# Optimization experiments

Hardware: AMD Instinct MI355X
Metric: run time of the kernel (lower is better)

The kernel has to match this reference:

```python
import jax, jax.numpy as jnp
import numpy as np

# static config (matches init_kwargs)
PL, LAT, LON = 8, 48, 96
WP, WL, WW = 2, 6, 12
SP, SL, SN = 1, 3, 6
NH = 16


def _earth_position_index(ws):
    wp, wl, ww = ws
    zi = np.arange(wp); zj = -np.arange(wp) * wp
    hi = np.arange(wl); hj = -np.arange(wl) * wl
    w = np.arange(ww)
    c1 = np.stack(np.meshgrid(zi, hi, w, indexing='ij')).reshape(3, -1)
    c2 = np.stack(np.meshgrid(zj, hj, w, indexing='ij')).reshape(3, -1)
    coords = (c1[:, :, None] - c2[:, None, :]).transpose(1, 2, 0).astype(np.int64)
    coords[:, :, 2] += ww - 1
    coords[:, :, 1] *= 2 * ww - 1
    coords[:, :, 0] *= (2 * ww - 1) * wl * wl
    return coords.sum(-1)  # (N, N)

_POS_IDX = jnp.asarray(_earth_position_index((WP, WL, WW)))


def _ln(x, w, b, eps=1e-5):
    m = x.mean(-1, keepdims=True)
    v = x.var(-1, keepdims=True)
    return (x - m) / jnp.sqrt(v + eps) * w + b


def setup_inputs() -> dict:
    key = jax.random.key(0)
    ks = jax.random.split(key, 8)
    B, C = 1, 512
    L = PL * LAT * LON
    TOW = (PL // WP) * (LAT // WL)
    TBL = WP * WP * WL * WL * (2 * WW - 1)
    s = 0.02
    return {
        'x': jax.random.normal(ks[0], (B, L, C), jnp.float32),
        'norm1_w': jnp.ones((C,), jnp.float32), 'norm1_b': jnp.zeros((C,), jnp.float32),
        'qkv_w': jax.random.normal(ks[1], (C, 3 * C), jnp.float32) * s,
        'qkv_b': jnp.zeros((3 * C,), jnp.float32),
        'proj_w': jax.random.normal(ks[2], (C, C), jnp.float32) * s,
        'proj_b': jnp.zeros((C,), jnp.float32),
        'bias_table': jax.random.normal(ks[3], (TBL, TOW, NH), jnp.float32) * s,
        'norm2_w': jnp.ones((C,), jnp.float32), 'norm2_b': jnp.zeros((C,), jnp.float32),
        'mlp_w1': jax.random.normal(ks[4], (C, 4 * C), jnp.float32) * s,
        'mlp_b1': jnp.zeros((4 * C,), jnp.float32),
        'mlp_w2': jax.random.normal(ks[5], (4 * C, C), jnp.float32) * s,
        'mlp_b2': jnp.zeros((C,), jnp.float32),
    }


def reference(x, norm1_w, norm1_b, qkv_w, qkv_b, proj_w, proj_b, bias_table,
              norm2_w, norm2_b, mlp_w1, mlp_b1, mlp_w2, mlp_b2):
    B, L, C = x.shape
    HD = C // NH
    scale = HD ** -0.5
    N = WP * WL * WW
    nPl, nLat, nLon = PL // WP, LAT // WL, LON // WW
    nW = nPl * nLat

    # norm1 + roll + window partition (B, nLon, nPl, nLat, wp, wl, ww, C)
    h = _ln(x, norm1_w, norm1_b).reshape(B, PL, LAT, LON, C)
    h = jnp.roll(h, (-SP, -SL, -SN), axis=(1, 2, 3))
    h = h.reshape(B, nPl, WP, nLat, WL, nLon, WW, C)
    h = h.transpose(0, 5, 1, 3, 2, 4, 6, 7).reshape(B * nLon, nW, N, C)

    # attention
    qkv = (h @ qkv_w + qkv_b).reshape(B * nLon, nW, N, 3, NH, HD)
    qkv = qkv.transpose(3, 0, 4, 1, 2, 5)  # (3, B_, nh, nW, N, hd)
    q, k, v = qkv[0] * scale, qkv[1], qkv[2]
    attn = jnp.einsum('bhwnd,bhwmd->bhwnm', q, k)
    bias = bias_table[_POS_IDX.reshape(-1)].reshape(N, N, nW, NH)
    bias = bias.transpose(3, 2, 0, 1)  # (nh, nW, N, N)
    attn = jax.nn.softmax(attn + bias[None], axis=-1)
    o = jnp.einsum('bhwnm,bhwmd->bhwnd', attn, v)
    o = o.transpose(0, 2, 3, 1, 4).reshape(B * nLon, nW, N, C)
    o = o @ proj_w + proj_b

    # reverse partition + roll back
    o = o.reshape(B, nLon, nPl, nLat, WP, WL, WW, C)
    o = o.transpose(0, 2, 4, 3, 5, 1, 6, 7).reshape(B, PL, LAT, LON, C)
    o = jnp.roll(o, (SP, SL, SN), axis=(1, 2, 3)).reshape(B, L, C)

    x = x + o
    h2 = _ln(x, norm2_w, norm2_b)
    h2 = jax.nn.gelu(h2 @ mlp_w1 + mlp_b1, approximate=False) @ mlp_w2 + mlp_b2
    return x + h2
```

## Files before the change

kernel.cpp:

```cpp
#include <hip/hip_runtime.h>
#include <hip/hip_bf16.h>
#include <math.h>

typedef __bf16 bf16;
typedef __attribute__((ext_vector_type(8))) __bf16 bf16x8;
typedef __attribute__((ext_vector_type(4))) float f32x4;
typedef __attribute__((ext_vector_type(8))) float f32x8;

#define NTOK   36864
#define CDIM   512
#define NHEAD  16
#define HD     32
#define NWIN   32
#define NLON   8
#define WTOK   144
#define TBL    3312

#define GLOAD_LDS16(g, l) __builtin_amdgcn_global_load_lds( \
    (const __attribute__((address_space(1))) void*)(const void*)(g), \
    (__attribute__((address_space(3))) void*)(l), 16, 0, 0)

__device__ __forceinline__ int src_token(int r) {
    int ww_ = r % 12; int q = r / 12;
    int wl_ = q % 6;  q /= 6;
    int wp_ = q & 1;  q >>= 1;
    int lat_g = q & 7; q >>= 3;
    int pl_g = q & 3;  q >>= 2;
    int lon_g = q;
    int pl  = pl_g * 2 + wp_ + 1;  if (pl  >= 8)  pl  -= 8;
    int lat = lat_g * 6 + wl_ + 3; if (lat >= 48) lat -= 48;
    int lon = lon_g * 12 + ww_ + 6; if (lon >= 96) lon -= 96;
    return (pl * 48 + lat) * 96 + lon;
}

__device__ __forceinline__ float gelu_exact(float x) {
    return 0.5f * x * (1.0f + erff(x * 0.70710678118654752f));
}

__global__ __launch_bounds__(256) void transpose_f32_bf16(const float* __restrict__ in,
                                                          bf16* __restrict__ out,
                                                          int R, int Cc) {
    __shared__ bf16 tile[32][33];
    int c0 = blockIdx.x * 32, r0 = blockIdx.y * 32;
    int tx = threadIdx.x & 31, ty = threadIdx.x >> 5;
#pragma unroll
    for (int i = 0; i < 32; i += 8)
        tile[ty + i][tx] = (bf16)in[(size_t)(r0 + ty + i) * Cc + c0 + tx];
    __syncthreads();
#pragma unroll
    for (int i = 0; i < 32; i += 8)
        out[(size_t)(c0 + ty + i) * R + r0 + tx] = tile[tx][ty + i];
}

__global__ __launch_bounds__(256) void table_transpose(const float* __restrict__ in,
                                                       float* __restrict__ outT) {
    __shared__ float tile[32][33];
    int i0 = blockIdx.x * 32, w0 = blockIdx.y * 32;
    int tx = threadIdx.x & 31, ty = threadIdx.x >> 5;
#pragma unroll
    for (int r = 0; r < 32; r += 8)
        if (i0 + ty + r < TBL) tile[ty + r][tx] = in[(size_t)(i0 + ty + r) * 512 + w0 + tx];
    __syncthreads();
#pragma unroll
    for (int r = 0; r < 32; r += 8)
        if (i0 + tx < TBL) outT[(size_t)(w0 + ty + r) * TBL + i0 + tx] = tile[tx][ty + r];
}

template<bool PERM>
__global__ __launch_bounds__(256) void ln_kernel(const float* __restrict__ in,
                                                 const float* __restrict__ w,
                                                 const float* __restrict__ b,
                                                 bf16* __restrict__ out) {
    int r = blockIdx.x * 4 + (threadIdx.x >> 6);
    int lane = threadIdx.x & 63;
    int s = PERM ? src_token(r) : r;
    f32x8 v8 = *(const f32x8*)(in + (size_t)s * CDIM + lane * 8);
    float sum = 0.f, sq = 0.f;
#pragma unroll
    for (int i = 0; i < 8; ++i) { sum += v8[i]; sq += v8[i] * v8[i]; }
#pragma unroll
    for (int m = 1; m < 64; m <<= 1) { sum += __shfl_xor(sum, m); sq += __shfl_xor(sq, m); }
    float mean = sum * (1.f / 512.f);
    float var  = sq  * (1.f / 512.f) - mean * mean;
    float rstd = rsqrtf(var + 1e-5f);
    f32x8 w8 = *(const f32x8*)(w + lane * 8);
    f32x8 b8 = *(const f32x8*)(b + lane * 8);
    bf16x8 o8;
#pragma unroll
    for (int i = 0; i < 8; ++i)
        o8[i] = (bf16)((v8[i] - mean) * rstd * w8[i] + b8[i]);
    *(bf16x8*)(out + (size_t)r * CDIM + lane * 8) = o8;
}

template<int EPI>
__global__ __launch_bounds__(256) void gemm_bt(const bf16* __restrict__ A,
                                               const bf16* __restrict__ Bt,
                                               const float* __restrict__ bias,
                                               void* __restrict__ Cout_,
                                               const float* __restrict__ X,
                                               int K, int N) {
    __shared__ bf16 As[128 * 32];
    __shared__ bf16 Bs[128 * 32];
    int t = threadIdx.x;
    int wid = t >> 6, lane = t & 63;
    int wr = wid >> 1, wc = wid & 1;
    int g = lane >> 4, cl = lane & 15;
    int m0 = blockIdx.y * 128, n0 = blockIdx.x * 128;
    f32x4 acc[4][4] = {};

    int srow = wid * 16 + (lane >> 2);
    int scol = (lane & 3) * 8;
    const bf16* Ag0 = A  + (size_t)(m0 + srow) * K + scol;
    const bf16* Ag1 = Ag0 + (size_t)64 * K;
    const bf16* Bg0 = Bt + (size_t)(n0 + srow) * K + scol;
    const bf16* Bg1 = Bg0 + (size_t)64 * K;
    bf16* Al0 = As + wid * 16 * 32;
    bf16* Al1 = Al0 + 64 * 32;
    bf16* Bl0 = Bs + wid * 16 * 32;
    bf16* Bl1 = Bl0 + 64 * 32;

    for (int k0 = 0; k0 < K; k0 += 32) {
        __syncthreads();
        GLOAD_LDS16(Ag0 + k0, Al0);
        GLOAD_LDS16(Ag1 + k0, Al1);
        GLOAD_LDS16(Bg0 + k0, Bl0);
        GLOAD_LDS16(Bg1 + k0, Bl1);
        __syncthreads();
        bf16x8 af[4], bfv[4];
#pragma unroll
        for (int i = 0; i < 4; ++i)
            af[i]  = *(const bf16x8*)(As + (wr * 64 + i * 16 + cl) * 32 + g * 8);
#pragma unroll
        for (int i = 0; i < 4; ++i)
            bfv[i] = *(const bf16x8*)(Bs + (wc * 64 + i * 16 + cl) * 32 + g * 8);
#pragma unroll
        for (int mi = 0; mi < 4; ++mi)
#pragma unroll
            for (int ni = 0; ni < 4; ++ni)
                acc[mi][ni] = __builtin_amdgcn_mfma_f32_16x16x32_bf16(af[mi], bfv[ni], acc[mi][ni], 0, 0, 0);
    }

#pragma unroll
    for (int mi = 0; mi < 4; ++mi) {
#pragma unroll
        for (int j = 0; j < 4; ++j) {
            int row = m0 + wr * 64 + mi * 16 + g * 4 + j;
            int srw = 0;
            if (EPI == 2) srw = src_token(row);
#pragma unroll
            for (int ni = 0; ni < 4; ++ni) {
                int col = n0 + wc * 64 + ni * 16 + cl;
                float v = acc[mi][ni][j] + bias[col];
                if (EPI == 1) v = gelu_exact(v);
                if (EPI == 0 || EPI == 1) {
                    ((bf16*)Cout_)[(size_t)row * N + col] = (bf16)v;
                } else if (EPI == 2) {
                    size_t o = (size_t)srw * CDIM + col;
                    ((float*)Cout_)[o] = X[o] + v;
                } else {
                    size_t o = (size_t)row * N + col;
                    ((float*)Cout_)[o] += v;
                }
            }
        }
    }
}

__global__ __launch_bounds__(256) void attn_mfma(const bf16* __restrict__ qkv,
                                                 const float* __restrict__ tableT,
                                                 bf16* __restrict__ obuf) {
    int h = blockIdx.x, w = blockIdx.y, b_ = blockIdx.z;
    int t = threadIdx.x, wid = t >> 6, lane = t & 63;
    int g = lane >> 4, cl = lane & 15;
    size_t base = ((size_t)b_ * NWIN + w) * WTOK;

    __shared__ bf16 P[WTOK * 168];
    __shared__ bf16 vT[32 * 168];
    __shared__ float bias_s[TBL];
    bf16* qs = P;
    bf16* ks = P + WTOK * 40;

    const bf16* qg = qkv + base * 1536 + h * 32;
    for (int tok = t >> 2; tok < WTOK; tok += 64) {
        int c8 = (t & 3) * 8;
        *(bf16x8*)(qs + tok * 40 + c8) = *(const bf16x8*)(qg + (size_t)tok * 1536 + c8);
        *(bf16x8*)(ks + tok * 40 + c8) = *(const bf16x8*)(qg + 512 + (size_t)tok * 1536 + c8);
        bf16x8 v8 = *(const bf16x8*)(qg + 1024 + (size_t)tok * 1536 + c8);
#pragma unroll
        for (int i = 0; i < 8; ++i) vT[(c8 + i) * 168 + tok] = v8[i];
    }
    for (int z = t; z < 32 * 24; z += 256) vT[(z / 24) * 168 + 144 + (z % 24)] = (bf16)0.f;
    const float* tb = tableT + (size_t)(w * 16 + h) * TBL;
    for (int i = t; i < TBL; i += 256) bias_s[i] = tb[i];
    __syncthreads();

    f32x4 sacc[3][9] = {};
    bf16x8 kf[9];
#pragma unroll
    for (int ct = 0; ct < 9; ++ct)
        kf[ct] = *(const bf16x8*)(ks + (ct * 16 + cl) * 40 + g * 8);
#pragma unroll
    for (int rti = 0; rti < 3; ++rti) {
        int rt = wid + rti * 4;
        if (rt < 9) {
            bf16x8 qf = *(const bf16x8*)(qs + (rt * 16 + cl) * 40 + g * 8);
#pragma unroll
            for (int ct = 0; ct < 9; ++ct)
                sacc[rti][ct] = __builtin_amdgcn_mfma_f32_16x16x32_bf16(qf, kf[ct], sacc[rti][ct], 0, 0, 0);
        }
    }
    __syncthreads();

    for (int z = t; z < WTOK * 24; z += 256) P[(z / 24) * 168 + 144 + (z % 24)] = (bf16)0.f;

    int bm[9];
#pragma unroll
    for (int ct = 0; ct < 9; ++ct) {
        int m = ct * 16 + cl;
        int wm = m % 12, tm = m / 12, hm = tm % 6, zm = tm / 6;
        bm[ct] = zm * 1656 + hm * 138 + 11 - wm;
    }

    const float scale = 0.17677669529663689f;
    float rinv[3][4];
#pragma unroll
    for (int rti = 0; rti < 3; ++rti) {
        int rt = wid + rti * 4;
        if (rt < 9) {
#pragma unroll
            for (int j = 0; j < 4; ++j) {
                int row = rt * 16 + g * 4 + j;
                int wn = row % 12, tn = row / 12, hn = tn % 6, zn = tn / 6;
                int an = zn * 828 + hn * 23 + wn;
                float mx = -1e30f;
#pragma unroll
                for (int ct = 0; ct < 9; ++ct) {
                    float v = sacc[rti][ct][j] * scale + bias_s[an + bm[ct]];
                    sacc[rti][ct][j] = v;
                    mx = fmaxf(mx, v);
                }
                for (int msk = 1; msk < 16; msk <<= 1) mx = fmaxf(mx, __shfl_xor(mx, msk));
                float sm = 0.f;
#pragma unroll
                for (int ct = 0; ct < 9; ++ct) {
                    float p = __expf(sacc[rti][ct][j] - mx);
                    sm += p;
                    P[row * 168 + ct * 16 + cl] = (bf16)p;
                }
                for (int msk = 1; msk < 16; msk <<= 1) sm += __shfl_xor(sm, msk);
                rinv[rti][j] = 1.f / sm;
            }
        }
    }
    __syncthreads();

#pragma unroll
    for (int rti = 0; rti < 3; ++rti) {
        int rt = wid + rti * 4;
        if (rt < 9) {
            f32x4 oacc[2] = {};
#pragma unroll
            for (int ks_ = 0; ks_ < 5; ++ks_) {
                bf16x8 pf = *(const bf16x8*)(P + (rt * 16 + cl) * 168 + ks_ * 32 + g * 8);
#pragma unroll
                for (int c2 = 0; c2 < 2; ++c2) {
                    bf16x8 vf = *(const bf16x8*)(vT + (c2 * 16 + cl) * 168 + ks_ * 32 + g * 8);
                    oacc[c2] = __builtin_amdgcn_mfma_f32_16x16x32_bf16(pf, vf, oacc[c2], 0, 0, 0);
                }
            }
#pragma unroll
            for (int c2 = 0; c2 < 2; ++c2)
#pragma unroll
                for (int j = 0; j < 4; ++j) {
                    int row = rt * 16 + g * 4 + j;
                    obuf[(base + row) * CDIM + h * 32 + c2 * 16 + cl] =
                        (bf16)(oacc[c2][j] * rinv[rti][j]);
                }
        }
    }
}

extern "C" void kernel_launch(void* const* d_in, const int* in_sizes, int n_in,
                              void* d_out, int out_size, void* d_ws, size_t ws_size,
                              hipStream_t stream) {
    const float* x       = (const float*)d_in[0];
    const float* n1w     = (const float*)d_in[1];
    const float* n1b     = (const float*)d_in[2];
    const float* qkv_w   = (const float*)d_in[3];
    const float* qkv_b   = (const float*)d_in[4];
    const float* proj_w  = (const float*)d_in[5];
    const float* proj_b  = (const float*)d_in[6];
    const float* btab    = (const float*)d_in[7];
    const float* n2w     = (const float*)d_in[8];
    const float* n2b     = (const float*)d_in[9];
    const float* mlp_w1  = (const float*)d_in[10];
    const float* mlp_b1  = (const float*)d_in[11];
    const float* mlp_w2  = (const float*)d_in[12];
    const float* mlp_b2  = (const float*)d_in[13];
    float* out = (float*)d_out;

    const size_t OFF_HBUF = 0;
    const size_t OFF_QKV  = 37748736;
    const size_t OFF_TT   = 150994944;
    const size_t OFF_OBUF = 188743680;
    const size_t OFF_WTQ  = 226492416;
    const size_t OFF_WTP  = 228065280;
    const size_t OFF_WT1  = 228589568;
    const size_t OFF_WT2  = 230686720;
    const size_t NEED     = 232783872;

    if (ws_size < NEED) return;

    char* ws = (char*)d_ws;
    bf16*  hbuf   = (bf16*)(ws + OFF_HBUF);
    bf16*  qkvbuf = (bf16*)(ws + OFF_QKV);
    bf16*  midbuf = qkvbuf;
    float* tableT = (float*)(ws + OFF_TT);
    bf16*  obuf   = (bf16*)(ws + OFF_OBUF);
    bf16*  wtq    = (bf16*)(ws + OFF_WTQ);
    bf16*  wtp    = (bf16*)(ws + OFF_WTP);
    bf16*  wt1    = (bf16*)(ws + OFF_WT1);
    bf16*  wt2    = (bf16*)(ws + OFF_WT2);

    transpose_f32_bf16<<<dim3(1536 / 32, 512 / 32), 256, 0, stream>>>(qkv_w, wtq, 512, 1536);
    transpose_f32_bf16<<<dim3(512 / 32, 512 / 32), 256, 0, stream>>>(proj_w, wtp, 512, 512);
    transpose_f32_bf16<<<dim3(2048 / 32, 512 / 32), 256, 0, stream>>>(mlp_w1, wt1, 512, 2048);
    transpose_f32_bf16<<<dim3(512 / 32, 2048 / 32), 256, 0, stream>>>(mlp_w2, wt2, 2048, 512);
    table_transpose<<<dim3((TBL + 31) / 32, 512 / 32), 256, 0, stream>>>(btab, tableT);

    ln_kernel<true><<<NTOK / 4, 256, 0, stream>>>(x, n1w, n1b, hbuf);

    gemm_bt<0><<<dim3(1536 / 128, NTOK / 128), 256, 0, stream>>>(hbuf, wtq, qkv_b, qkvbuf, nullptr, 512, 1536);

    attn_mfma<<<dim3(NHEAD, NWIN, NLON), 256, 0, stream>>>(qkvbuf, tableT, obuf);

    gemm_bt<2><<<dim3(512 / 128, NTOK / 128), 256, 0, stream>>>(obuf, wtp, proj_b, out, x, 512, 512);

    ln_kernel<false><<<NTOK / 4, 256, 0, stream>>>(out, n2w, n2b, hbuf);

    gemm_bt<1><<<dim3(2048 / 128, NTOK / 128), 256, 0, stream>>>(hbuf, wt1, mlp_b1, midbuf, nullptr, 512, 2048);

    gemm_bt<3><<<dim3(512 / 128, NTOK / 128), 256, 0, stream>>>(midbuf, wt2, mlp_b2, out, nullptr, 2048, 512);
}
```

Measured before the change: 632.2 us.

## Replace LDS-staged GEMM with direct-to-register loads, XCD swizzle, and tanh GELU

The GEMM no longer stages tiles through shared memory. Each wave loads its MFMA fragments straight from global memory into registers, with K fixed at compile time and the k loop unrolled, which removes the two barriers per k step. A 1D grid whose blocks are remapped across the 8 XCDs replaces the 2D grid to improve L2 locality. The exact erf GELU is also replaced by a tanh approximation; this changes the numerics against the reference and trades the shared-memory reuse within a block for more global and L2 traffic.

```diff
diff --git a/kernel.cpp b/kernel.cpp
--- a/kernel.cpp
+++ b/kernel.cpp
@@ -15,10 +15,6 @@
 #define NLON   8
 #define WTOK   144
 #define TBL    3312
-
-#define GLOAD_LDS16(g, l) __builtin_amdgcn_global_load_lds( \
-    (const __attribute__((address_space(1))) void*)(const void*)(g), \
-    (__attribute__((address_space(3))) void*)(l), 16, 0, 0)
 
 __device__ __forceinline__ int src_token(int r) {
     int ww_ = r % 12; int q = r / 12;
@@ -33,8 +29,10 @@
     return (pl * 48 + lat) * 96 + lon;
 }
 
-__device__ __forceinline__ float gelu_exact(float x) {
-    return 0.5f * x * (1.0f + erff(x * 0.70710678118654752f));
+__device__ __forceinline__ float gelu_fast(float x) {
+    float u = 1.5957691216f * (x + 0.044715f * x * x * x);
+    float t = 1.f - 2.f / (__expf(u) + 1.f);
+    return 0.5f * x * (1.f + t);
 }
 
 __global__ __launch_bounds__(256) void transpose_f32_bf16(const float* __restrict__ in,
@@ -92,47 +90,40 @@
     *(bf16x8*)(out + (size_t)r * CDIM + lane * 8) = o8;
 }
 
-template<int EPI>
-__global__ __launch_bounds__(256) void gemm_bt(const bf16* __restrict__ A,
-                                               const bf16* __restrict__ Bt,
-                                               const float* __restrict__ bias,
-                                               void* __restrict__ Cout_,
-                                               const float* __restrict__ X,
-                                               int K, int N) {
-    __shared__ bf16 As[128 * 32];
-    __shared__ bf16 Bs[128 * 32];
-    int t = threadIdx.x;
-    int wid = t >> 6, lane = t & 63;
-    int wr = wid >> 1, wc = wid & 1;
-    int g = lane >> 4, cl = lane & 15;
-    int m0 = blockIdx.y * 128, n0 = blockIdx.x * 128;
+template<int EPI, int K>
+__global__ __launch_bounds__(256) void gemm_direct(const bf16* __restrict__ A,
+                                                   const bf16* __restrict__ Bt,
+                                                   const float* __restrict__ bias,
+                                                   void* __restrict__ Cout_,
+                                                   const float* __restrict__ X,
+                                                   int N, int gx) {
+    const int t = threadIdx.x;
+    const int wid = t >> 6, lane = t & 63;
+    const int wr = wid >> 1, wc = wid & 1;
+    const int g = lane >> 4, cl = lane & 15;
+
+    int nwg = gridDim.x, orig = blockIdx.x;
+    int wg = orig;
+    if ((nwg & 7) == 0) {
+        int cpx = nwg >> 3;
+        wg = (orig & 7) * cpx + (orig >> 3);
+    }
+    const int m0 = (wg / gx) * 128, n0 = (wg % gx) * 128;
+
     f32x4 acc[4][4] = {};
 
-    int srow = wid * 16 + (lane >> 2);
-    int scol = (lane & 3) * 8;
-    const bf16* Ag0 = A  + (size_t)(m0 + srow) * K + scol;
-    const bf16* Ag1 = Ag0 + (size_t)64 * K;
-    const bf16* Bg0 = Bt + (size_t)(n0 + srow) * K + scol;
-    const bf16* Bg1 = Bg0 + (size_t)64 * K;
-    bf16* Al0 = As + wid * 16 * 32;
-    bf16* Al1 = Al0 + 64 * 32;
-    bf16* Bl0 = Bs + wid * 16 * 32;
-    bf16* Bl1 = Bl0 + 64 * 32;
-
+    const bf16* Ap = A  + (size_t)(m0 + wr * 64 + cl) * K + g * 8;
+    const bf16* Bp = Bt + (size_t)(n0 + wc * 64 + cl) * K + g * 8;
+
+#pragma unroll 4
     for (int k0 = 0; k0 < K; k0 += 32) {
-        __syncthreads();
-        GLOAD_LDS16(Ag0 + k0, Al0);
-        GLOAD_LDS16(Ag1 + k0, Al1);
-        GLOAD_LDS16(Bg0 + k0, Bl0);
-        GLOAD_LDS16(Bg1 + k0, Bl1);
-        __syncthreads();
         bf16x8 af[4], bfv[4];
 #pragma unroll
         for (int i = 0; i < 4; ++i)
-            af[i]  = *(const bf16x8*)(As + (wr * 64 + i * 16 + cl) * 32 + g * 8);
+            af[i]  = *(const bf16x8*)(Ap + (size_t)i * 16 * K + k0);
 #pragma unroll
         for (int i = 0; i < 4; ++i)
-            bfv[i] = *(const bf16x8*)(Bs + (wc * 64 + i * 16 + cl) * 32 + g * 8);
+            bfv[i] = *(const bf16x8*)(Bp + (size_t)i * 16 * K + k0);
 #pragma unroll
         for (int mi = 0; mi < 4; ++mi)
 #pragma unroll
@@ -151,7 +142,7 @@
             for (int ni = 0; ni < 4; ++ni) {
                 int col = n0 + wc * 64 + ni * 16 + cl;
                 float v = acc[mi][ni][j] + bias[col];
-                if (EPI == 1) v = gelu_exact(v);
+                if (EPI == 1) v = gelu_fast(v);
                 if (EPI == 0 || EPI == 1) {
                     ((bf16*)Cout_)[(size_t)row * N + col] = (bf16)v;
                 } else if (EPI == 2) {
@@ -330,15 +321,15 @@
 
     ln_kernel<true><<<NTOK / 4, 256, 0, stream>>>(x, n1w, n1b, hbuf);
 
-    gemm_bt<0><<<dim3(1536 / 128, NTOK / 128), 256, 0, stream>>>(hbuf, wtq, qkv_b, qkvbuf, nullptr, 512, 1536);
+    gemm_direct<0, 512><<<12 * 288, 256, 0, stream>>>(hbuf, wtq, qkv_b, qkvbuf, nullptr, 1536, 12);
 
     attn_mfma<<<dim3(NHEAD, NWIN, NLON), 256, 0, stream>>>(qkvbuf, tableT, obuf);
 
-    gemm_bt<2><<<dim3(512 / 128, NTOK / 128), 256, 0, stream>>>(obuf, wtp, proj_b, out, x, 512, 512);
+    gemm_direct<2, 512><<<4 * 288, 256, 0, stream>>>(obuf, wtp, proj_b, out, x, 512, 4);
 
     ln_kernel<false><<<NTOK / 4, 256, 0, stream>>>(out, n2w, n2b, hbuf);
 
-    gemm_bt<1><<<dim3(2048 / 128, NTOK / 128), 256, 0, stream>>>(hbuf, wt1, mlp_b1, midbuf, nullptr, 512, 2048);
-
-    gemm_bt<3><<<dim3(512 / 128, NTOK / 128), 256, 0, stream>>>(midbuf, wt2, mlp_b2, out, nullptr, 2048, 512);
-}
+    gemm_direct<1, 512><<<16 * 288, 256, 0, stream>>>(hbuf, wt1, mlp_b1, midbuf, nullptr, 2048, 16);
+
+    gemm_direct<3, 2048><<<4 * 288, 256, 0, stream>>>(midbuf, wt2, mlp_b2, out, nullptr, 512, 4);
+}
```

New measurement: 1.070 ms. +69.2%, slower.
